# Optimization experiments

Measured on AMD Instinct MI355X. Metric: run time of the kernel, lower is better.

## Reference

```python
import jax, jax.numpy as jnp
import numpy as np


def setup_inputs() -> dict:
    key = jax.random.key(0)
    k1, k2, k3, k4 = jax.random.split(key, 4)
    N, D, B = 300000, 256, 512
    x = jax.random.normal(k1, (N, D), dtype=jnp.float32)
    batch = jnp.sort(jax.random.randint(k2, (N,), 0, B, dtype=jnp.int64))
    W1 = jax.random.normal(k3, (D, D // 2), dtype=jnp.float32) / np.sqrt(D)
    b1 = jnp.zeros((D // 2,), dtype=jnp.float32)
    W2 = jax.random.normal(k4, (D // 2, 1), dtype=jnp.float32) / np.sqrt(D // 2)
    b2 = jnp.zeros((1,), dtype=jnp.float32)
    return {"x": x, "batch": batch, "num_segments": B,
            "W1": W1, "b1": b1, "W2": W2, "b2": b2}


def reference(x, batch, num_segments, W1, b1, W2, b2):
    # attention MLP: Linear -> ReLU -> Linear, output [N, 1]
    h = jax.nn.relu(x @ W1 + b1)
    scores = h @ W2 + b2                       # [N, 1]
    # softmax over ALL nodes (dim=0), as in the original module
    w = jax.nn.softmax(scores, axis=0)          # [N, 1]
    # weighted segment-sum per graph; empty segments yield zero rows
    pooled = jax.ops.segment_sum(x * w, batch, num_segments=num_segments)
    return pooled                                # [num_segments, D]
```

## Files before the change

kernel.cpp:

```cpp
#include <hip/hip_runtime.h>
#include <math.h>

typedef __attribute__((ext_vector_type(8))) short bf16x8;
typedef __attribute__((ext_vector_type(4))) float f32x4;

constexpr int D = 256;
constexpr int H = 128;
constexpr int KSTEPS = D / 32;
constexpr int BM = 128;

__device__ __forceinline__ float trunc_bf(float a) {
  return __uint_as_float(__float_as_uint(a) & 0xFFFF0000u);
}
__device__ __forceinline__ unsigned int pack2_bf(float a, float b) {
  return (__float_as_uint(a) >> 16) | (__float_as_uint(b) & 0xFFFF0000u);
}

union FragU { uint4 u; bf16x8 f; };

__device__ __forceinline__ void gload16(const void* g, void* l) {
  __builtin_amdgcn_global_load_lds(
      (const __attribute__((address_space(1))) unsigned int*)g,
      (__attribute__((address_space(3))) unsigned int*)l, 16, 0, 0);
}
__device__ __forceinline__ void block_sync() {
  asm volatile("" ::: "memory");
  __builtin_amdgcn_s_barrier();
  asm volatile("" ::: "memory");
}

extern "C" __global__ void __launch_bounds__(256)
k_init(float* __restrict__ out, int out_size, float* __restrict__ zacc)
{
  const int i = blockIdx.x * 256 + threadIdx.x;
  if (i < out_size) out[i] = 0.0f;
  if (i == 0) *zacc = 0.0f;
}

extern "C" __global__ void __launch_bounds__(256)
k_pack(const float* __restrict__ W1, uint4* __restrict__ phi,
       uint4* __restrict__ plo)
{
  const int g = blockIdx.x * 256 + threadIdx.x;
  const int c = g >> 9, ht = (g >> 6) & 7, l = g & 63;
  const int kbase = c * 32 + (l >> 4) * 8;
  const int col = ht * 16 + (l & 15);
  float v[8], lo[8];
#pragma unroll
  for (int i = 0; i < 8; ++i) {
    v[i] = W1[(size_t)(kbase + i) * H + col];
    lo[i] = v[i] - trunc_bf(v[i]);
  }
  uint4 h4, l4;
  h4.x = pack2_bf(v[0], v[1]); h4.y = pack2_bf(v[2], v[3]);
  h4.z = pack2_bf(v[4], v[5]); h4.w = pack2_bf(v[6], v[7]);
  l4.x = pack2_bf(lo[0], lo[1]); l4.y = pack2_bf(lo[2], lo[3]);
  l4.z = pack2_bf(lo[4], lo[5]); l4.w = pack2_bf(lo[6], lo[7]);
  phi[g] = h4; plo[g] = l4;
}

extern "C" __global__ void __launch_bounds__(256, 3)
k_fused(const float* __restrict__ x, const int* __restrict__ batch,
        const uint4* __restrict__ phi, const uint4* __restrict__ plo,
        const float* __restrict__ b1, const float* __restrict__ W2,
        const float* __restrict__ b2, float* __restrict__ out,
        float* __restrict__ zacc, int N)
{
  __shared__ float4 xplane[2][1024];
  __shared__ float sred[2][BM];
  __shared__ float wlds[BM];

  const int t = threadIdx.x;
  const int l = t & 63;
  const int w = t >> 6;
  const int lg = l >> 4;
  const int lr = l & 15;
  const int rg = w >> 1;
  const int cg = w & 1;
  const int n0 = blockIdx.x * BM;

  const char* xb = (const char*)x;

  auto STAGE = [&](int buf, int c) {
#pragma unroll
    for (int i = 0; i < 4; ++i) {
      const int plane = i * 4 + w;
      const int g = plane >> 1, p = plane & 1;
      const int srow = min(n0 + g * 16 + lr, N - 1);
      gload16(xb + (size_t)srow * 1024 + c * 128 + lg * 32 + p * 16,
              (char*)&xplane[buf][plane * 64 + l]);
    }
  };

  f32x4 acc[4][4] = {};

  STAGE(0, 0);
#pragma unroll 1
  for (int c = 0; c < KSTEPS; ++c) {
    const int cur = c & 1;
    FragU bhi[4], blo[4];
#pragma unroll
    for (int h = 0; h < 4; ++h) {
      const int ht = cg * 4 + h;
      bhi[h].u = phi[(c * 8 + ht) * 64 + l];
      blo[h].u = plo[(c * 8 + ht) * 64 + l];
    }
    if (c + 1 < KSTEPS) {
      STAGE(cur ^ 1, c + 1);
      asm volatile("s_waitcnt vmcnt(4)" ::: "memory");
    } else {
      asm volatile("s_waitcnt vmcnt(0)" ::: "memory");
    }
    block_sync();

#pragma unroll
    for (int s = 0; s < 4; ++s) {
      const int g = rg * 4 + s;
      const float4 u0 = xplane[cur][(g * 2 + 0) * 64 + l];
      const float4 u1 = xplane[cur][(g * 2 + 1) * 64 + l];
      float v[8], lo[8];
      v[0] = u0.x; v[1] = u0.y; v[2] = u0.z; v[3] = u0.w;
      v[4] = u1.x; v[5] = u1.y; v[6] = u1.z; v[7] = u1.w;
#pragma unroll
      for (int i = 0; i < 8; ++i) lo[i] = v[i] - trunc_bf(v[i]);
      FragU ahi, alo;
      ahi.u.x = pack2_bf(v[0], v[1]);  ahi.u.y = pack2_bf(v[2], v[3]);
      ahi.u.z = pack2_bf(v[4], v[5]);  ahi.u.w = pack2_bf(v[6], v[7]);
      alo.u.x = pack2_bf(lo[0], lo[1]); alo.u.y = pack2_bf(lo[2], lo[3]);
      alo.u.z = pack2_bf(lo[4], lo[5]); alo.u.w = pack2_bf(lo[6], lo[7]);
#pragma unroll
      for (int h = 0; h < 4; ++h) {
        acc[s][h] = __builtin_amdgcn_mfma_f32_16x16x32_bf16(ahi.f, bhi[h].f, acc[s][h], 0, 0, 0);
        acc[s][h] = __builtin_amdgcn_mfma_f32_16x16x32_bf16(ahi.f, blo[h].f, acc[s][h], 0, 0, 0);
        acc[s][h] = __builtin_amdgcn_mfma_f32_16x16x32_bf16(alo.f, bhi[h].f, acc[s][h], 0, 0, 0);
      }
    }
    block_sync();
  }

  float bvv[4], wvv[4];
#pragma unroll
  for (int h = 0; h < 4; ++h) {
    const int col = (cg * 4 + h) * 16 + lr;
    bvv[h] = b1[col];
    wvv[h] = W2[col];
  }
#pragma unroll
  for (int s = 0; s < 4; ++s) {
#pragma unroll
    for (int r = 0; r < 4; ++r) {
      float p = 0.0f;
#pragma unroll
      for (int h = 0; h < 4; ++h)
        p = fmaf(fmaxf(acc[s][h][r] + bvv[h], 0.0f), wvv[h], p);
#pragma unroll
      for (int off = 1; off < 16; off <<= 1) p += __shfl_xor(p, off, 64);
      if (lr == 0) sred[cg][rg * 64 + s * 16 + lg * 4 + r] = p;
    }
  }
  __syncthreads();
  if (cg == 0) {
    const int row = rg * 64 + l;
    const int node = n0 + row;
    const float sc = sred[0][row] + sred[1][row] + b2[0];
    const float wgt = (node < N) ? __expf(sc) : 0.0f;
    wlds[row] = wgt;
    float zs = wgt;
#pragma unroll
    for (int off = 1; off < 64; off <<= 1) zs += __shfl_xor(zs, off, 64);
    if (l == 0) atomicAdd(zacc, zs);
  }
  __syncthreads();

  {
    const int nStart = n0 + w * 32;
    const int nEnd = min(nStart + 32, N);
    if (nStart < nEnd) {
      float4 a4 = make_float4(0.f, 0.f, 0.f, 0.f);
      int bprev = batch[nStart];
      for (int n = nStart; n < nEnd; ++n) {
        const int b = batch[n];
        if (b != bprev) {
          float* o = out + (size_t)bprev * D + l * 4;
          atomicAdd(o + 0, a4.x); atomicAdd(o + 1, a4.y);
          atomicAdd(o + 2, a4.z); atomicAdd(o + 3, a4.w);
          a4 = make_float4(0.f, 0.f, 0.f, 0.f);
          bprev = b;
        }
        const float wgt = wlds[n - n0];
        const float4 xv = *reinterpret_cast<const float4*>(x + (size_t)n * D + l * 4);
        a4.x = fmaf(xv.x, wgt, a4.x);
        a4.y = fmaf(xv.y, wgt, a4.y);
        a4.z = fmaf(xv.z, wgt, a4.z);
        a4.w = fmaf(xv.w, wgt, a4.w);
      }
      float* o = out + (size_t)bprev * D + l * 4;
      atomicAdd(o + 0, a4.x); atomicAdd(o + 1, a4.y);
      atomicAdd(o + 2, a4.z); atomicAdd(o + 3, a4.w);
    }
  }
}

extern "C" __global__ void __launch_bounds__(256)
k_finish(float* __restrict__ out, const float* __restrict__ zacc, int size)
{
  const int i = blockIdx.x * 256 + threadIdx.x;
  if (i < size) out[i] *= (1.0f / *zacc);
}

extern "C" void kernel_launch(void* const* d_in, const int* in_sizes, int n_in,
                              void* d_out, int out_size, void* d_ws, size_t ws_size,
                              hipStream_t stream)
{
  const float* x     = (const float*)d_in[0];
  const int*   batch = (const int*)d_in[1];
  const float* W1 = (const float*)d_in[3];
  const float* b1 = (const float*)d_in[4];
  const float* W2 = (const float*)d_in[5];
  const float* b2 = (const float*)d_in[6];
  const int N = in_sizes[1];

  float* zacc = (float*)d_ws;
  uint4* phi  = (uint4*)((char*)d_ws + 256);
  uint4* plo  = (uint4*)((char*)d_ws + 256 + 65536);

  k_init<<<(out_size + 255) / 256, 256, 0, stream>>>((float*)d_out, out_size, zacc);
  k_pack<<<16, 256, 0, stream>>>(W1, phi, plo);

  const int g1 = (N + BM - 1) / BM;
  k_fused<<<g1, 256, 0, stream>>>(x, batch, phi, plo, b1, W2, b2,
                                  (float*)d_out, zacc, N);

  k_finish<<<(out_size + 255) / 256, 256, 0, stream>>>((float*)d_out, zacc, out_size);
}
```

Measured before the change: 181.6 us.

## Preload whole bf16-split x tile into swizzled LDS, drop per-step barriers

New measurement: 205.1 us. +13.0%, slower.

```diff
diff --git a/kernel.cpp b/kernel.cpp
--- a/kernel.cpp
+++ b/kernel.cpp
@@ -7,7 +7,7 @@
 constexpr int D = 256;
 constexpr int H = 128;
 constexpr int KSTEPS = D / 32;
-constexpr int BM = 128;
+constexpr int BM = 64;
 
 __device__ __forceinline__ float trunc_bf(float a) {
   return __uint_as_float(__float_as_uint(a) & 0xFFFF0000u);
@@ -17,17 +17,6 @@
 }
 
 union FragU { uint4 u; bf16x8 f; };
-
-__device__ __forceinline__ void gload16(const void* g, void* l) {
-  __builtin_amdgcn_global_load_lds(
-      (const __attribute__((address_space(1))) unsigned int*)g,
-      (__attribute__((address_space(3))) unsigned int*)l, 16, 0, 0);
-}
-__device__ __forceinline__ void block_sync() {
-  asm volatile("" ::: "memory");
-  __builtin_amdgcn_s_barrier();
-  asm volatile("" ::: "memory");
-}
 
 extern "C" __global__ void __launch_bounds__(256)
 k_init(float* __restrict__ out, int out_size, float* __restrict__ zacc)
@@ -59,14 +48,18 @@
   phi[g] = h4; plo[g] = l4;
 }
 
-extern "C" __global__ void __launch_bounds__(256, 3)
-k_fused(const float* __restrict__ x, const int* __restrict__ batch,
-        const uint4* __restrict__ phi, const uint4* __restrict__ plo,
-        const float* __restrict__ b1, const float* __restrict__ W2,
-        const float* __restrict__ b2, float* __restrict__ out,
-        float* __restrict__ zacc, int N)
-{
-  __shared__ float4 xplane[2][1024];
+__device__ __forceinline__ int slot_of(int lg, int r15, int c) {
+  return lg * 16 + (r15 ^ ((lg + 2 * c) & 15));
+}
+
+extern "C" __global__ void __launch_bounds__(256, 2)
+k_fused2(const float* __restrict__ x, const int* __restrict__ batch,
+         const uint4* __restrict__ phi, const uint4* __restrict__ plo,
+         const float* __restrict__ b1, const float* __restrict__ W2,
+         const float* __restrict__ b2, float* __restrict__ out,
+         float* __restrict__ zacc, int N)
+{
+  __shared__ char xlds[KSTEPS * 4 * 2048];
   __shared__ float sred[2][BM];
   __shared__ float wlds[BM];
 
@@ -79,55 +72,56 @@
   const int cg = w & 1;
   const int n0 = blockIdx.x * BM;
 
-  const char* xb = (const char*)x;
-
-  auto STAGE = [&](int buf, int c) {
-#pragma unroll
-    for (int i = 0; i < 4; ++i) {
-      const int plane = i * 4 + w;
-      const int g = plane >> 1, p = plane & 1;
-      const int srow = min(n0 + g * 16 + lr, N - 1);
-      gload16(xb + (size_t)srow * 1024 + c * 128 + lg * 32 + p * 16,
-              (char*)&xplane[buf][plane * 64 + l]);
-    }
-  };
-
-  f32x4 acc[4][4] = {};
-
-  STAGE(0, 0);
+  {
+    const int wc = l >> 3;
+    const int wlg = (l >> 1) & 3;
+    const int wp = l & 1;
+#pragma unroll
+    for (int i = 0; i < 16; ++i) {
+      const int row = w * 16 + i;
+      const int srow = min(n0 + row, N - 1);
+      const float4 v = *reinterpret_cast<const float4*>(x + (size_t)srow * D + l * 4);
+      uint2 hi, lo;
+      hi.x = pack2_bf(v.x, v.y);
+      hi.y = pack2_bf(v.z, v.w);
+      lo.x = pack2_bf(v.x - trunc_bf(v.x), v.y - trunc_bf(v.y));
+      lo.y = pack2_bf(v.z - trunc_bf(v.z), v.w - trunc_bf(v.w));
+      const int sl = slot_of(wlg, row & 15, wc);
+      char* pb = xlds + (wc * 4 + (row >> 4)) * 2048 + sl * 16 + wp * 8;
+      *reinterpret_cast<uint2*>(pb) = hi;
+      *reinterpret_cast<uint2*>(pb + 1024) = lo;
+    }
+  }
+
+  FragU bhi[4], blo[4], nbhi[4], nblo[4];
+#pragma unroll
+  for (int h = 0; h < 4; ++h) {
+    const int ht = cg * 4 + h;
+    bhi[h].u = phi[(0 * 8 + ht) * 64 + l];
+    blo[h].u = plo[(0 * 8 + ht) * 64 + l];
+  }
+  __syncthreads();
+
+  f32x4 acc[2][4] = {};
+
 #pragma unroll 1
   for (int c = 0; c < KSTEPS; ++c) {
-    const int cur = c & 1;
-    FragU bhi[4], blo[4];
-#pragma unroll
-    for (int h = 0; h < 4; ++h) {
-      const int ht = cg * 4 + h;
-      bhi[h].u = phi[(c * 8 + ht) * 64 + l];
-      blo[h].u = plo[(c * 8 + ht) * 64 + l];
-    }
     if (c + 1 < KSTEPS) {
-      STAGE(cur ^ 1, c + 1);
-      asm volatile("s_waitcnt vmcnt(4)" ::: "memory");
-    } else {
-      asm volatile("s_waitcnt vmcnt(0)" ::: "memory");
-    }
-    block_sync();
-
-#pragma unroll
-    for (int s = 0; s < 4; ++s) {
-      const int g = rg * 4 + s;
-      const float4 u0 = xplane[cur][(g * 2 + 0) * 64 + l];
-      const float4 u1 = xplane[cur][(g * 2 + 1) * 64 + l];
-      float v[8], lo[8];
-      v[0] = u0.x; v[1] = u0.y; v[2] = u0.z; v[3] = u0.w;
-      v[4] = u1.x; v[5] = u1.y; v[6] = u1.z; v[7] = u1.w;
-#pragma unroll
-      for (int i = 0; i < 8; ++i) lo[i] = v[i] - trunc_bf(v[i]);
+#pragma unroll
+      for (int h = 0; h < 4; ++h) {
+        const int ht = cg * 4 + h;
+        nbhi[h].u = phi[((c + 1) * 8 + ht) * 64 + l];
+        nblo[h].u = plo[((c + 1) * 8 + ht) * 64 + l];
+      }
+    }
+    const int sl = slot_of(lg, lr, c);
+#pragma unroll
+    for (int s = 0; s < 2; ++s) {
+      const int g = rg * 2 + s;
+      const char* pb = xlds + (c * 4 + g) * 2048 + sl * 16;
       FragU ahi, alo;
-      ahi.u.x = pack2_bf(v[0], v[1]);  ahi.u.y = pack2_bf(v[2], v[3]);
-      ahi.u.z = pack2_bf(v[4], v[5]);  ahi.u.w = pack2_bf(v[6], v[7]);
-      alo.u.x = pack2_bf(lo[0], lo[1]); alo.u.y = pack2_bf(lo[2], lo[3]);
-      alo.u.z = pack2_bf(lo[4], lo[5]); alo.u.w = pack2_bf(lo[6], lo[7]);
+      ahi.f = *reinterpret_cast<const bf16x8*>(pb);
+      alo.f = *reinterpret_cast<const bf16x8*>(pb + 1024);
 #pragma unroll
       for (int h = 0; h < 4; ++h) {
         acc[s][h] = __builtin_amdgcn_mfma_f32_16x16x32_bf16(ahi.f, bhi[h].f, acc[s][h], 0, 0, 0);
@@ -135,7 +129,8 @@
         acc[s][h] = __builtin_amdgcn_mfma_f32_16x16x32_bf16(alo.f, bhi[h].f, acc[s][h], 0, 0, 0);
       }
     }
-    block_sync();
+#pragma unroll
+    for (int h = 0; h < 4; ++h) { bhi[h] = nbhi[h]; blo[h] = nblo[h]; }
   }
 
   float bvv[4], wvv[4];
@@ -146,7 +141,7 @@
     wvv[h] = W2[col];
   }
 #pragma unroll
-  for (int s = 0; s < 4; ++s) {
+  for (int s = 0; s < 2; ++s) {
 #pragma unroll
     for (int r = 0; r < 4; ++r) {
       float p = 0.0f;
@@ -155,16 +150,16 @@
         p = fmaf(fmaxf(acc[s][h][r] + bvv[h], 0.0f), wvv[h], p);
 #pragma unroll
       for (int off = 1; off < 16; off <<= 1) p += __shfl_xor(p, off, 64);
-      if (lr == 0) sred[cg][rg * 64 + s * 16 + lg * 4 + r] = p;
+      if (lr == 0) sred[cg][rg * 32 + s * 16 + lg * 4 + r] = p;
     }
   }
   __syncthreads();
   if (cg == 0) {
-    const int row = rg * 64 + l;
+    const int row = rg * 32 + (l & 31);
     const int node = n0 + row;
     const float sc = sred[0][row] + sred[1][row] + b2[0];
-    const float wgt = (node < N) ? __expf(sc) : 0.0f;
-    wlds[row] = wgt;
+    const float wgt = (l < 32 && node < N) ? __expf(sc) : 0.0f;
+    if (l < 32) wlds[row] = wgt;
     float zs = wgt;
 #pragma unroll
     for (int off = 1; off < 64; off <<= 1) zs += __shfl_xor(zs, off, 64);
@@ -173,8 +168,8 @@
   __syncthreads();
 
   {
-    const int nStart = n0 + w * 32;
-    const int nEnd = min(nStart + 32, N);
+    const int nStart = n0 + w * 16;
+    const int nEnd = min(nStart + 16, N);
     if (nStart < nEnd) {
       float4 a4 = make_float4(0.f, 0.f, 0.f, 0.f);
       int bprev = batch[nStart];
@@ -228,8 +223,8 @@
   k_pack<<<16, 256, 0, stream>>>(W1, phi, plo);
 
   const int g1 = (N + BM - 1) / BM;
-  k_fused<<<g1, 256, 0, stream>>>(x, batch, phi, plo, b1, W2, b2,
-                                  (float*)d_out, zacc, N);
+  k_fused2<<<g1, 256, 0, stream>>>(x, batch, phi, plo, b1, W2, b2,
+                                   (float*)d_out, zacc, N);
 
   k_finish<<<(out_size + 255) / 256, 256, 0, stream>>>((float*)d_out, zacc, out_size);
 }
```
